# Kernel optimization log

Hardware: AMD Instinct MI355X
Metric: run time of the kernel (lower is better)

## Reference

```python
import jax, jax.numpy as jnp
import numpy as np
from jax import lax

B, N, D = 2, 2048, 256
S, DC, E = 16, 4, 2
DI = E * D            # d_inner = 512
DTR = (D + 15) // 16  # dt_rank = 16


def layernorm(x, w, b):
    m = x.mean(-1, keepdims=True)
    v = ((x - m) ** 2).mean(-1, keepdims=True)
    return (x - m) / jnp.sqrt(v + 1e-5) * w + b


def mamba_block(x, in_w, conv_w, conv_b, xproj_w, dt_w, dt_b, A_log, Dp, out_w):
    # x: [B, N, D]
    xz = jnp.einsum('bnd,ed->bne', x, in_w)          # [B,N,2*DI]
    xc, z = jnp.split(xz, 2, axis=-1)
    # depthwise causal conv1d, kernel DC, left-pad DC-1
    xpad = jnp.pad(xc, ((0, 0), (DC - 1, 0), (0, 0)))
    xconv = sum(xpad[:, k:k + N, :] * conv_w[:, k] for k in range(DC)) + conv_b
    xa = jax.nn.silu(xconv)                           # [B,N,DI]
    x_dbl = jnp.einsum('bnd,ed->bne', xa, xproj_w)    # [B,N,DTR+2S]
    dt = x_dbl[..., :DTR]
    Bm = x_dbl[..., DTR:DTR + S]                      # [B,N,S]
    Cm = x_dbl[..., DTR + S:]                         # [B,N,S]
    dt = jax.nn.softplus(jnp.einsum('bnr,dr->bnd', dt, dt_w) + dt_b)  # [B,N,DI]
    A = -jnp.exp(A_log)                               # [DI,S]
    dA = jnp.exp(dt[..., None] * A)                   # [B,N,DI,S]
    dBu = dt[..., None] * Bm[:, :, None, :] * xa[..., None]

    def step(h, inp):
        dA_t, dBu_t, C_t = inp
        h = dA_t * h + dBu_t                          # [B,DI,S]
        y = jnp.einsum('bds,bs->bd', h, C_t)
        return h, y

    h0 = jnp.zeros((x.shape[0], DI, S), dtype=x.dtype)
    _, ys = lax.scan(step, h0, (dA.transpose(1, 0, 2, 3), dBu.transpose(1, 0, 2, 3), Cm.transpose(1, 0, 2)))
    y = ys.transpose(1, 0, 2) + xa * Dp               # skip D*u
    y = y * jax.nn.silu(z)
    return jnp.einsum('bnd,ed->bne', y, out_w)        # [B,N,D]


def stream_fwd(x, nw, nb, in_w, conv_w, conv_b, xproj_w, dt_w, dt_b, A_log, Dp, out_w):
    return x + mamba_block(layernorm(x, nw, nb), in_w, conv_w, conv_b, xproj_w, dt_w, dt_b, A_log, Dp, out_w)


def setup_inputs() -> dict:
    key = jax.random.key(0)
    ks = jax.random.split(key, 24)
    s = 0.02
    inp = {
        'edge_features': jax.random.normal(ks[0], (B, N, D), jnp.float32),
        'blob_features': jax.random.normal(ks[1], (B, N, D), jnp.float32),
        'spectral_features': jax.random.normal(ks[2], (B, N, D), jnp.float32),
        'norm_w': jnp.ones((3, D)),
        'norm_b': jnp.zeros((3, D)),
        'in_w': jax.random.normal(ks[3], (3, 2 * DI, D)) * s,
        'conv_w': jax.random.normal(ks[4], (3, DI, DC)) * s,
        'conv_b': jnp.zeros((3, DI)),
        'xproj_w': jax.random.normal(ks[5], (3, DTR + 2 * S, DI)) * s,
        'dt_w': jax.random.normal(ks[6], (3, DI, DTR)) * s,
        'dt_b': jax.random.uniform(ks[7], (3, DI), minval=-4.0, maxval=-2.0),
        'A_log': jnp.tile(jnp.log(jnp.arange(1, S + 1, dtype=jnp.float32)), (3, DI, 1)),
        'Dp': jnp.ones((3, DI)),
        'out_w': jax.random.normal(ks[8], (3, D, DI)) * s,
        'temperature': jnp.ones((1,)) * 0.1,
        'agg_w1': jax.random.normal(ks[9], (D, 3 * D)) * s,
        'agg_b1': jnp.zeros((D,)),
        'agg_w2': jax.random.normal(ks[10], (3, D)) * s,
        'agg_b2': jnp.zeros((3,)),
        'proj_w': jax.random.normal(ks[11], (D, 3 * D)) * s,
        'proj_b': jnp.zeros((D,)),
    }
    return inp


def reference(edge_features, blob_features, spectral_features, norm_w, norm_b, in_w,
              conv_w, conv_b, xproj_w, dt_w, dt_b, A_log, Dp, out_w, temperature,
              agg_w1, agg_b1, agg_w2, agg_b2, proj_w, proj_b):
    streams = jnp.stack([edge_features, blob_features, spectral_features])  # [3,B,N,D]
    proc = jax.vmap(stream_fwd)(streams, norm_w, norm_b, in_w, conv_w, conv_b,
                                xproj_w, dt_w, dt_b, A_log, Dp, out_w)      # [3,B,N,D]
    edge_p, blob_p, spec_p = proc[0], proc[1], proc[2]
    multi = jnp.concatenate([edge_p, blob_p, spec_p], axis=-1)              # [B,N,3D]
    pooled = multi.mean(axis=1, keepdims=True)                              # [B,1,3D]
    h = jax.nn.gelu(jnp.einsum('bne,de->bnd', pooled, agg_w1) + agg_b1)
    coeffs = jax.nn.softmax(jnp.einsum('bnd,kd->bnk', h, agg_w2) + agg_b2, axis=-1)
    coeffs = jax.nn.softmax(coeffs / (temperature + 1e-6), axis=-1)         # [B,1,3]
    weighted = (coeffs[:, :, 0:1] * edge_p + coeffs[:, :, 1:2] * blob_p +
                coeffs[:, :, 2:3] * spec_p)
    out = jnp.einsum('bne,de->bnd', multi, proj_w) + proj_b + weighted
    return out  # dropout is identity in eval
```

## Files before the change

kernel.cpp:

```cpp
#include <hip/hip_runtime.h>
#include <hip/hip_bf16.h>

#define NB 2
#define NN 2048
#define ND 256
#define NS 16
#define NDC 4
#define NDI 512
#define NDTR 16
#define LCH 32
#define NCH 64

typedef __hip_bfloat16 bf16;
typedef __attribute__((ext_vector_type(8))) __bf16 bf16x8;
typedef __attribute__((ext_vector_type(4))) float f32x4;

__device__ __forceinline__ float b2f(bf16 h) { return __bfloat162float(h); }

__device__ __forceinline__ void dec8(const uint4 u, float w[8]) {
    union { unsigned u; float f; } c;
    c.u = u.x << 16;          w[0] = c.f;
    c.u = u.x & 0xffff0000u;  w[1] = c.f;
    c.u = u.y << 16;          w[2] = c.f;
    c.u = u.y & 0xffff0000u;  w[3] = c.f;
    c.u = u.z << 16;          w[4] = c.f;
    c.u = u.z & 0xffff0000u;  w[5] = c.f;
    c.u = u.w << 16;          w[6] = c.f;
    c.u = u.w & 0xffff0000u;  w[7] = c.f;
}

struct CvtArgs { const void* s[21]; };
__device__ __constant__ const int seg_cum[22] = {
    0, 1048576, 2097152, 3145728, 3146496, 3147264, 3933696, 3939840,
    3941376, 4015104, 4039680, 4041216, 4065792, 4067328, 4460544, 4460545,
    4657153, 4657409, 4658177, 4658180, 4854788, 4855044 };
__device__ __constant__ const int seg_dst[21] = {
    0,        1048576,  2097152,  4847616, 4848384, 3145728, 4841472, 4849152, 4325376,
    4399104,  4850688,  4423680,  4852224, 3932160, 4855056, 4448256, 4853760, 4854016,
    4854784,  4644864,  4854800 };

__global__ __launch_bounds__(256) void k_convert(CvtArgs a, int* __restrict__ flag,
                                                 bf16* __restrict__ dst,
                                                 float* __restrict__ pooled)
{
    int idx0 = blockIdx.x * 256 + threadIdx.x;
    unsigned v0 = ((const unsigned*)a.s[3])[0];
    int f = ((v0 & 0xFFFFu) == 0u) ? 1 : 0;
    if (idx0 == 0) flag[0] = f;
    if (idx0 < 1536) pooled[idx0] = 0.0f;
    int idx = idx0 + 3145728;
    if (idx >= 4855044) return;
    int seg = 3;
    #pragma unroll
    for (int i = 4; i < 21; i++) if (idx >= seg_cum[i]) seg = i;
    int off = idx - seg_cum[seg];
    bf16 v;
    if (f) v = __float2bfloat16(((const float*)a.s[seg])[off]);
    else   v = ((const bf16*)a.s[seg])[off];
    dst[seg_dst[seg] + off] = v;
}

__global__ __launch_bounds__(256) void k_ln(
    const void* __restrict__ e, const void* __restrict__ bl, const void* __restrict__ sp,
    const void* __restrict__ nw_raw, const void* __restrict__ nb_raw,
    bf16* __restrict__ cvt_in,
    bf16* __restrict__ xn)
{
    int row = blockIdx.x;
    int sb = row >> 11, n = row & (NN - 1);
    int s = sb >> 1, b = sb & 1;
    int t = threadIdx.x;
    unsigned v0 = ((const unsigned*)nw_raw)[0];
    int f = ((v0 & 0xFFFFu) == 0u);
    const void* xin = (s == 0) ? e : ((s == 1) ? bl : sp);
    size_t gi = ((size_t)(b << 11) + n) * ND + t;
    float v = f ? ((const float*)xin)[gi] : b2f(((const bf16*)xin)[gi]);
    cvt_in[(size_t)s * 1048576 + gi] = __float2bfloat16(v);
    float s1 = v, s2 = v * v;
    #pragma unroll
    for (int m = 1; m < 64; m <<= 1) { s1 += __shfl_xor(s1, m); s2 += __shfl_xor(s2, m); }
    __shared__ float r1[4], r2[4];
    int w = t >> 6;
    if ((t & 63) == 0) { r1[w] = s1; r2[w] = s2; }
    __syncthreads();
    float mean = (r1[0] + r1[1] + r1[2] + r1[3]) * (1.0f / ND);
    float ms   = (r2[0] + r2[1] + r2[2] + r2[3]) * (1.0f / ND);
    float inv = rsqrtf(ms - mean * mean + 1e-5f);
    float wv = f ? ((const float*)nw_raw)[s * ND + t] : b2f(((const bf16*)nw_raw)[s * ND + t]);
    float bv = f ? ((const float*)nb_raw)[s * ND + t] : b2f(((const bf16*)nb_raw)[s * ND + t]);
    xn[(size_t)row * ND + t] = __float2bfloat16((v - mean) * inv * wv + bv);
}

__global__ __launch_bounds__(256) void k_inproj_t(
    const bf16* __restrict__ xn, const bf16* __restrict__ in_w,
    bf16* __restrict__ xc, bf16* __restrict__ z)
{
    __shared__ bf16 As[128 * 72];
    __shared__ bf16 Bs[128 * 72];
    int bid = blockIdx.x;
    int bm = bid >> 3, bn = bid & 7;
    int m0 = bm * 128, e0 = bn * 128;
    int s = m0 >> 12;
    const bf16* W = in_w + (size_t)s * (2 * NDI) * ND;
    int t = threadIdx.x;
    int w = t >> 6, l = t & 63;
    int wm = w >> 1, wn = w & 1;
    int quad = l >> 4, lan = l & 15;
    f32x4 acc[4][4];
    #pragma unroll
    for (int mi = 0; mi < 4; mi++)
        #pragma unroll
        for (int j = 0; j < 4; j++) acc[mi][j] = (f32x4){0.f, 0.f, 0.f, 0.f};
    for (int kc0 = 0; kc0 < 256; kc0 += 64) {
        __syncthreads();
        #pragma unroll
        for (int i = 0; i < 4; i++) {
            int li = i * 256 + t;
            int row = li >> 3, col = (li & 7) * 8;
            *(uint4*)&As[row * 72 + col] =
                *(const uint4*)(xn + (size_t)(m0 + row) * ND + kc0 + col);
        }
        #pragma unroll
        for (int i = 0; i < 4; i++) {
            int li = i * 256 + t;
            int row = li >> 3, col = (li & 7) * 8;
            *(uint4*)&Bs[row * 72 + col] =
                *(const uint4*)(W + (size_t)(e0 + row) * ND + kc0 + col);
        }
        __syncthreads();
        #pragma unroll
        for (int kc = 0; kc < 64; kc += 32) {
            bf16x8 af[4], bf[4];
            #pragma unroll
            for (int mi = 0; mi < 4; mi++)
                af[mi] = *(const bf16x8*)&As[(wm * 64 + mi * 16 + lan) * 72 + kc + quad * 8];
            #pragma unroll
            for (int j = 0; j < 4; j++)
                bf[j] = *(const bf16x8*)&Bs[(wn * 64 + j * 16 + lan) * 72 + kc + quad * 8];
            #pragma unroll
            for (int mi = 0; mi < 4; mi++)
                #pragma unroll
                for (int j = 0; j < 4; j++)
                    acc[mi][j] = __builtin_amdgcn_mfma_f32_16x16x32_bf16(af[mi], bf[j], acc[mi][j], 0, 0, 0);
        }
    }
    #pragma unroll
    for (int mi = 0; mi < 4; mi++) {
        #pragma unroll
        for (int j = 0; j < 4; j++) {
            int e = e0 + wn * 64 + j * 16 + lan;
            bf16* dst = (e < NDI) ? xc : z;
            int ec = e & (NDI - 1);
            #pragma unroll
            for (int r = 0; r < 4; r++) {
                int m = m0 + wm * 64 + mi * 16 + quad * 4 + r;
                dst[(size_t)m * NDI + ec] = __float2bfloat16(acc[mi][j][r]);
            }
        }
    }
}

__global__ __launch_bounds__(256) void k_conv(
    const bf16* __restrict__ xc, const bf16* __restrict__ conv_w,
    const bf16* __restrict__ conv_b, bf16* __restrict__ xa)
{
    int idx = blockIdx.x * 256 + threadIdx.x;
    int d8 = (idx & 63) * 8;
    int rn = idx >> 6;
    int n = rn & (NN - 1);
    int sb = rn >> 11;
    int s = sb >> 1;
    const uint4* cwp = (const uint4*)(conv_w + ((size_t)s * NDI + d8) * NDC);
    float cwf[32];
    dec8(cwp[0], cwf); dec8(cwp[1], cwf + 8); dec8(cwp[2], cwf + 16); dec8(cwp[3], cwf + 24);
    float bias[8];
    dec8(*(const uint4*)(conv_b + (size_t)s * NDI + d8), bias);
    size_t g = (size_t)rn * NDI + d8;
    float xv[4][8];
    #pragma unroll
    for (int tau = 0; tau < 4; tau++) {
        if (n >= tau) dec8(*(const uint4*)(xc + g - (size_t)tau * NDI), xv[tau]);
        else
            #pragma unroll
            for (int j = 0; j < 8; j++) xv[tau][j] = 0.0f;
    }
    union { bf16 h[8]; uint4 u; } o;
    #pragma unroll
    for (int j = 0; j < 8; j++) {
        float a = bias[j];
        #pragma unroll
        for (int k = 0; k < 4; k++) a += cwf[j * 4 + k] * xv[3 - k][j];
        a = a / (1.0f + __expf(-a));
        o.h[j] = __float2bfloat16(a);
    }
    *(uint4*)(xa + g) = o.u;
}

__global__ __launch_bounds__(256) void k_xproj_t(
    const bf16* __restrict__ xa, const bf16* __restrict__ xproj_w,
    float* __restrict__ xpart)
{
    __shared__ bf16 As[64 * 72];
    __shared__ bf16 Bs[48 * 72];
    int bid = blockIdx.x;
    int bm = bid >> 2, ks = bid & 3;
    int m0 = bm * 64;
    int s = m0 >> 12;
    const bf16* W = xproj_w + (size_t)s * 48 * NDI;
    int t = threadIdx.x;
    int w = t >> 6, l = t & 63;
    int quad = l >> 4, lan = l & 15;
    f32x4 acc[3];
    #pragma unroll
    for (int j = 0; j < 3; j++) acc[j] = (f32x4){0.f, 0.f, 0.f, 0.f};
    for (int kc0 = ks * 128; kc0 < ks * 128 + 128; kc0 += 64) {
        __syncthreads();
        #pragma unroll
        for (int i = 0; i < 2; i++) {
            int li = i * 256 + t;
            int row = li >> 3, col = (li & 7) * 8;
            *(uint4*)&As[row * 72 + col] =
                *(const uint4*)(xa + (size_t)(m0 + row) * NDI + kc0 + col);
        }
        {
            int li = t;
            if (li < 384) {
                int row = li >> 3, col = (li & 7) * 8;
                *(uint4*)&Bs[row * 72 + col] =
                    *(const uint4*)(W + (size_t)row * NDI + kc0 + col);
            }
            int li2 = 256 + t;
            if (li2 < 384) {
                int row = li2 >> 3, col = (li2 & 7) * 8;
                *(uint4*)&Bs[row * 72 + col] =
                    *(const uint4*)(W + (size_t)row * NDI + kc0 + col);
            }
        }
        __syncthreads();
        #pragma unroll
        for (int kc = 0; kc < 64; kc += 32) {
            bf16x8 af = *(const bf16x8*)&As[(w * 16 + lan) * 72 + kc + quad * 8];
            #pragma unroll
            for (int j = 0; j < 3; j++) {
                bf16x8 bf = *(const bf16x8*)&Bs[(j * 16 + lan) * 72 + kc + quad * 8];
                acc[j] = __builtin_amdgcn_mfma_f32_16x16x32_bf16(af, bf, acc[j], 0, 0, 0);
            }
        }
    }
    float* dst = xpart + (size_t)ks * (12288 * 48);
    #pragma unroll
    for (int j = 0; j < 3; j++) {
        int e = j * 16 + lan;
        #pragma unroll
        for (int r = 0; r < 4; r++) {
            int m = m0 + w * 16 + quad * 4 + r;
            dst[(size_t)m * 48 + e] = acc[j][r];
        }
    }
}

__global__ __launch_bounds__(256) void k_dt2(
    const float* __restrict__ xpart, const bf16* __restrict__ dt_w,
    const bf16* __restrict__ dt_b, float* __restrict__ xdbl, bf16* __restrict__ dt)
{
    __shared__ float xs[4][48];
    int row0 = blockIdx.x * 4;
    int s = row0 >> 12;
    int t = threadIdx.x;
    if (t < 192) {
        int r = t / 48, e = t % 48;
        size_t base = (size_t)(row0 + r) * 48 + e;
        const size_t seg = (size_t)12288 * 48;
        float v = xpart[base] + xpart[base + seg] + xpart[base + 2 * seg] + xpart[base + 3 * seg];
        xs[r][e] = v;
        if (e >= 16) xdbl[base] = v;
    }
    __syncthreads();
    #pragma unroll
    for (int dd = 0; dd < 2; dd++) {
        int d = t + dd * 256;
        const uint4* wp = (const uint4*)(dt_w + ((size_t)s * NDI + d) * NDTR);
        float w[16]; dec8(wp[0], w); dec8(wp[1], w + 8);
        float bias = b2f(dt_b[s * NDI + d]);
        #pragma unroll
        for (int r = 0; r < 4; r++) {
            float a = bias;
            #pragma unroll
            for (int j = 0; j < 16; j++) a += w[j] * xs[r][j];
            a = (a > 20.0f) ? a : log1pf(__expf(a));
            dt[(size_t)(row0 + r) * NDI + d] = __float2bfloat16(a);
        }
    }
}

__global__ __launch_bounds__(256) void k_scan1(
    const bf16* __restrict__ dt, const bf16* __restrict__ xa,
    const bf16* __restrict__ A_log, const float* __restrict__ xdbl,
    float* __restrict__ Hend, float* __restrict__ Pprod)
{
    __shared__ bf16 dts[LCH * 256];
    __shared__ bf16 xas[LCH * 256];
    __shared__ float Bs[LCH * NS];
    int bid = blockIdx.x;
    int sb = bid / (NCH * 2);
    int rem = bid % (NCH * 2);
    int chunk = rem >> 1, dg = rem & 1;
    int s = sb >> 1;
    int t = threadIdx.x;
    int d = dg * 256 + t;
    int n0 = chunk * LCH;
    size_t rowbase = (size_t)sb * NN;
    const bf16* dtg = dt + (rowbase + n0) * NDI + dg * 256;
    const bf16* xag = xa + (rowbase + n0) * NDI + dg * 256;
    #pragma unroll
    for (int i = 0; i < 4; i++) {
        int li = i * 256 + t;
        int row = li >> 5, q = li & 31;
        ((uint4*)dts)[li] = *(const uint4*)(dtg + (size_t)row * NDI + q * 8);
        ((uint4*)xas)[li] = *(const uint4*)(xag + (size_t)row * NDI + q * 8);
    }
    if (t < 128) {
        int row = t >> 2, q = t & 3;
        ((float4*)Bs)[t] = ((const float4*)(xdbl + (rowbase + n0 + row) * 48 + 16))[q];
    }
    float A[16];
    {
        const uint4* ap = (const uint4*)(A_log + ((size_t)s * NDI + d) * NS);
        float al[8]; dec8(ap[0], al);
        #pragma unroll
        for (int i = 0; i < 8; i++) A[i] = -__expf(al[i]);
        dec8(ap[1], al);
        #pragma unroll
        for (int i = 0; i < 8; i++) A[8 + i] = -__expf(al[i]);
    }
    __syncthreads();
    float h[16], P[16];
    #pragma unroll
    for (int i = 0; i < 16; i++) { h[i] = 0.0f; P[i] = 1.0f; }
    #pragma unroll 4
    for (int nl = 0; nl < LCH; nl++) {
        float dtv = b2f(dts[nl * 256 + t]);
        float xav = b2f(xas[nl * 256 + t]);
        float bcom = dtv * xav;
        const float4* br = (const float4*)&Bs[nl * NS];
        float4 b0 = br[0], b1 = br[1], b2 = br[2], b3 = br[3];
        float bv[16] = {b0.x,b0.y,b0.z,b0.w,b1.x,b1.y,b1.z,b1.w,
                        b2.x,b2.y,b2.z,b2.w,b3.x,b3.y,b3.z,b3.w};
        #pragma unroll
        for (int st = 0; st < 16; st++) {
            float dA = __expf(dtv * A[st]);
            h[st] = dA * h[st] + bcom * bv[st];
            P[st] *= dA;
        }
    }
    size_t base = ((size_t)(chunk * 6 + sb) * NS) * NDI + d;
    #pragma unroll
    for (int st = 0; st < 16; st++) {
        Hend[base + (size_t)st * NDI] = h[st];
        Pprod[base + (size_t)st * NDI] = P[st];
    }
}

__global__ __launch_bounds__(256) void k_scomb(float* __restrict__ Hend, const float* __restrict__ Pprod)
{
    int idx = blockIdx.x * 256 + threadIdx.x;
    int sb = idx >> 13;
    int rem = idx & 8191;
    int st = rem >> 9, d = rem & 511;
    float h = 0.0f;
    const size_t stride = (size_t)6 * NS * NDI;
    size_t g = ((size_t)sb * NS + st) * NDI + d;
    #pragma unroll 4
    for (int c = 0; c < NCH; c++) {
        float He = Hend[g], Pp = Pprod[g];
        Hend[g] = h;
        h = He + Pp * h;
        g += stride;
    }
}

__global__ __launch_bounds__(256) void k_scan2(
    const bf16* __restrict__ dt, const bf16* __restrict__ xa, const bf16* __restrict__ z,
    const float* __restrict__ xdbl,
    const bf16* __restrict__ A_log, const bf16* __restrict__ Dp,
    const float* __restrict__ Hstart, bf16* __restrict__ y)
{
    __shared__ bf16 dts[LCH * 256];
    __shared__ bf16 xas[LCH * 256];
    __shared__ bf16 zs[LCH * 256];
    __shared__ float Bs[LCH * NS], Cs[LCH * NS];
    int bid = blockIdx.x;
    int sb = bid / (NCH * 2);
    int rem = bid % (NCH * 2);
    int chunk = rem >> 1, dg = rem & 1;
    int s = sb >> 1;
    int t = threadIdx.x;
    int d = dg * 256 + t;
    int n0 = chunk * LCH;
    size_t rowbase = (size_t)sb * NN;
    const bf16* dtg = dt + (rowbase + n0) * NDI + dg * 256;
    const bf16* xag = xa + (rowbase + n0) * NDI + dg * 256;
    const bf16* zg  = z  + (rowbase + n0) * NDI + dg * 256;
    #pragma unroll
    for (int i = 0; i < 4; i++) {
        int li = i * 256 + t;
        int row = li >> 5, q = li & 31;
        ((uint4*)dts)[li] = *(const uint4*)(dtg + (size_t)row * NDI + q * 8);
        ((uint4*)xas)[li] = *(const uint4*)(xag + (size_t)row * NDI + q * 8);
        ((uint4*)zs)[li]  = *(const uint4*)(zg  + (size_t)row * NDI + q * 8);
    }
    if (t < 128) {
        int row = t >> 2, q = t & 3;
        ((float4*)Bs)[t] = ((const float4*)(xdbl + (rowbase + n0 + row) * 48 + 16))[q];
    } else {
        int t2 = t - 128;
        int row = t2 >> 2, q = t2 & 3;
        ((float4*)Cs)[t2] = ((const float4*)(xdbl + (rowbase + n0 + row) * 48 + 32))[q];
    }
    float A[16];
    {
        const uint4* ap = (const uint4*)(A_log + ((size_t)s * NDI + d) * NS);
        float al[8]; dec8(ap[0], al);
        #pragma unroll
        for (int i = 0; i < 8; i++) A[i] = -__expf(al[i]);
        dec8(ap[1], al);
        #pragma unroll
        for (int i = 0; i < 8; i++) A[8 + i] = -__expf(al[i]);
    }
    float Dpv = b2f(Dp[s * NDI + d]);
    float h[16];
    {
        size_t base = ((size_t)(chunk * 6 + sb) * NS) * NDI + d;
        #pragma unroll
        for (int st = 0; st < 16; st++) h[st] = Hstart[base + (size_t)st * NDI];
    }
    __syncthreads();
    bf16* yp = y + (rowbase + n0) * NDI + d;
    #pragma unroll 4
    for (int nl = 0; nl < LCH; nl++) {
        float dtv = b2f(dts[nl * 256 + t]);
        float xav = b2f(xas[nl * 256 + t]);
        float zz  = b2f(zs[nl * 256 + t]);
        float bcom = dtv * xav;
        const float4* br = (const float4*)&Bs[nl * NS];
        const float4* cr = (const float4*)&Cs[nl * NS];
        float4 b0 = br[0], b1 = br[1], b2 = br[2], b3 = br[3];
        float4 c0 = cr[0], c1 = cr[1], c2 = cr[2], c3 = cr[3];
        float bv[16] = {b0.x,b0.y,b0.z,b0.w,b1.x,b1.y,b1.z,b1.w,
                        b2.x,b2.y,b2.z,b2.w,b3.x,b3.y,b3.z,b3.w};
        float cv[16] = {c0.x,c0.y,c0.z,c0.w,c1.x,c1.y,c1.z,c1.w,
                        c2.x,c2.y,c2.z,c2.w,c3.x,c3.y,c3.z,c3.w};
        float yacc = 0.0f;
        #pragma unroll
        for (int st = 0; st < 16; st++) {
            float dA = __expf(dtv * A[st]);
            h[st] = dA * h[st] + bcom * bv[st];
            yacc += h[st] * cv[st];
        }
        float yv = yacc + xav * Dpv;
        yv *= zz / (1.0f + __expf(-zz));
        yp[(size_t)nl * NDI] = __float2bfloat16(yv);
    }
}

__global__ __launch_bounds__(256) void k_outproj_t(
    const bf16* __restrict__ y, const bf16* __restrict__ out_w,
    const bf16* __restrict__ e_, const bf16* __restrict__ bl, const bf16* __restrict__ sp,
    bf16* __restrict__ proc, float* __restrict__ pooled)
{
    __shared__ bf16 As[128 * 72];
    __shared__ bf16 Bs[64 * 72];
    __shared__ float colsum[64];
    int bid = blockIdx.x;
    int bm = bid >> 2, bn = bid & 3;
    int m0 = bm * 128, e0 = bn * 64;
    int s = m0 >> 12;
    const bf16* W = out_w + (size_t)s * ND * NDI;
    int t = threadIdx.x;
    int w = t >> 6, l = t & 63;
    int quad = l >> 4, lan = l & 15;
    f32x4 acc[2][4];
    #pragma unroll
    for (int mi = 0; mi < 2; mi++)
        #pragma unroll
        for (int j = 0; j < 4; j++) acc[mi][j] = (f32x4){0.f, 0.f, 0.f, 0.f};
    for (int kc0 = 0; kc0 < 512; kc0 += 64) {
        __syncthreads();
        #pragma unroll
        for (int i = 0; i < 4; i++) {
            int li = i * 256 + t;
            int row = li >> 3, col = (li & 7) * 8;
            *(uint4*)&As[row * 72 + col] =
                *(const uint4*)(y + (size_t)(m0 + row) * NDI + kc0 + col);
        }
        #pragma unroll
        for (int i = 0; i < 2; i++) {
            int li = i * 256 + t;
            int row = li >> 3, col = (li & 7) * 8;
            *(uint4*)&Bs[row * 72 + col] =
                *(const uint4*)(W + (size_t)(e0 + row) * NDI + kc0 + col);
        }
        __syncthreads();
        #pragma unroll
        for (int kc = 0; kc < 64; kc += 32) {
            bf16x8 af[2], bf[4];
            #pragma unroll
            for (int mi = 0; mi < 2; mi++)
                af[mi] = *(const bf16x8*)&As[(w * 32 + mi * 16 + lan) * 72 + kc + quad * 8];
            #pragma unroll
            for (int j = 0; j < 4; j++)
                bf[j] = *(const bf16x8*)&Bs[(j * 16 + lan) * 72 + kc + quad * 8];
            #pragma unroll
            for (int mi = 0; mi < 2; mi++)
                #pragma unroll
                for (int j = 0; j < 4; j++)
                    acc[mi][j] = __builtin_amdgcn_mfma_f32_16x16x32_bf16(af[mi], bf[j], acc[mi][j], 0, 0, 0);
        }
    }
    if (t < 64) colsum[t] = 0.0f;
    __syncthreads();
    const bf16* xin = (s == 0) ? e_ : ((s == 1) ? bl : sp);
    int b = (m0 >> 11) & 1;
    #pragma unroll
    for (int mi = 0; mi < 2; mi++) {
        #pragma unroll
        for (int j = 0; j < 4; j++) {
            int e = e0 + j * 16 + lan;
            float ps = 0.0f;
            #pragma unroll
            for (int r = 0; r < 4; r++) {
                int m = m0 + w * 32 + mi * 16 + quad * 4 + r;
                int n = m & (NN - 1);
                float v = acc[mi][j][r] + b2f(xin[((size_t)(b * NN + n)) * ND + e]);
                proc[(size_t)m * ND + e] = __float2bfloat16(v);
                ps += v;
            }
            atomicAdd(&colsum[j * 16 + lan], ps);
        }
    }
    __syncthreads();
    if (t < 64) atomicAdd(&pooled[b * 768 + s * 256 + e0 + t], colsum[t]);
}

__global__ __launch_bounds__(256) void k_final_t(
    const bf16* __restrict__ proc, const bf16* __restrict__ proj_w,
    const bf16* __restrict__ proj_b, const float* __restrict__ pooled,
    const bf16* __restrict__ agg_w1, const bf16* __restrict__ agg_b1,
    const bf16* __restrict__ agg_w2, const bf16* __restrict__ agg_b2,
    const bf16* __restrict__ temp,
    const int* __restrict__ flag, void* __restrict__ out)
{
    __shared__ bf16 As[128 * 72];
    __shared__ bf16 Bs[64 * 72];
    __shared__ float hb[256];
    __shared__ float lg[3];
    __shared__ float cf[3];
    int bid = blockIdx.x;
    int bm = bid >> 2, bn = bid & 3;
    int m0 = bm * 128, e0 = bn * 64;
    int b = m0 >> 11;
    int nbase = m0 & (NN - 1);
    int t = threadIdx.x;
    int w = t >> 6, l = t & 63;
    int quad = l >> 4, lan = l & 15;
    {
        float dot = 0.0f;
        const uint4* wp = (const uint4*)(agg_w1 + (size_t)t * 768);
        for (int k8 = 0; k8 < 96; k8++) {
            float wv[8]; dec8(wp[k8], wv);
            const float* pp = pooled + b * 768 + k8 * 8;
            #pragma unroll
            for (int j = 0; j < 8; j++) dot += wv[j] * pp[j];
        }
        float x = b2f(agg_b1[t]) + dot * (1.0f / NN);
        float inner = 0.7978845608028654f * (x + 0.044715f * x * x * x);
        hb[t] = 0.5f * x * (1.0f + tanhf(inner));
        __syncthreads();
        if (t < 3) {
            float ll = b2f(agg_b2[t]);
            const bf16* w2 = agg_w2 + t * 256;
            for (int d2 = 0; d2 < 256; d2++) ll += b2f(w2[d2]) * hb[d2];
            lg[t] = ll;
        }
        __syncthreads();
        if (t == 0) {
            float m = fmaxf(lg[0], fmaxf(lg[1], lg[2]));
            float e0f = __expf(lg[0] - m), e1 = __expf(lg[1] - m), e2 = __expf(lg[2] - m);
            float iS = 1.0f / (e0f + e1 + e2);
            float c0 = e0f * iS, c1 = e1 * iS, c2 = e2 * iS;
            float tt = b2f(temp[0]) + 1e-6f;
            float m2 = fmaxf(c0, fmaxf(c1, c2)) / tt;
            e0f = __expf(c0 / tt - m2); e1 = __expf(c1 / tt - m2); e2 = __expf(c2 / tt - m2);
            iS = 1.0f / (e0f + e1 + e2);
            cf[0] = e0f * iS; cf[1] = e1 * iS; cf[2] = e2 * iS;
        }
    }
    f32x4 acc[2][4];
    #pragma unroll
    for (int mi = 0; mi < 2; mi++)
        #pragma unroll
        for (int j = 0; j < 4; j++) acc[mi][j] = (f32x4){0.f, 0.f, 0.f, 0.f};
    for (int kc0 = 0; kc0 < 768; kc0 += 64) {
        int sA = kc0 >> 8, kd0 = kc0 & 255;
        const bf16* Asrc = proc + ((size_t)(sA * NB + b) * NN + nbase) * ND + kd0;
        __syncthreads();
        #pragma unroll
        for (int i = 0; i < 4; i++) {
            int li = i * 256 + t;
            int row = li >> 3, col = (li & 7) * 8;
            *(uint4*)&As[row * 72 + col] = *(const uint4*)(Asrc + (size_t)row * ND + col);
        }
        #pragma unroll
        for (int i = 0; i < 2; i++) {
            int li = i * 256 + t;
            int row = li >> 3, col = (li & 7) * 8;
            *(uint4*)&Bs[row * 72 + col] =
                *(const uint4*)(proj_w + (size_t)(e0 + row) * 768 + kc0 + col);
        }
        __syncthreads();
        #pragma unroll
        for (int kc = 0; kc < 64; kc += 32) {
            bf16x8 af[2], bf[4];
            #pragma unroll
            for (int mi = 0; mi < 2; mi++)
                af[mi] = *(const bf16x8*)&As[(w * 32 + mi * 16 + lan) * 72 + kc + quad * 8];
            #pragma unroll
            for (int j = 0; j < 4; j++)
                bf[j] = *(const bf16x8*)&Bs[(j * 16 + lan) * 72 + kc + quad * 8];
            #pragma unroll
            for (int mi = 0; mi < 2; mi++)
                #pragma unroll
                for (int j = 0; j < 4; j++)
                    acc[mi][j] = __builtin_amdgcn_mfma_f32_16x16x32_bf16(af[mi], bf[j], acc[mi][j], 0, 0, 0);
        }
    }
    float c0 = cf[0], c1 = cf[1], c2 = cf[2];
    int f = flag[0];
    #pragma unroll
    for (int mi = 0; mi < 2; mi++) {
        #pragma unroll
        for (int j = 0; j < 4; j++) {
            int e = e0 + j * 16 + lan;
            float pb = b2f(proj_b[e]);
            #pragma unroll
            for (int r = 0; r < 4; r++) {
                int m = m0 + w * 32 + mi * 16 + quad * 4 + r;
                int n = m & (NN - 1);
                size_t pbase = ((size_t)b * NN + n) * ND + e;
                float wres = c0 * b2f(proc[pbase])
                           + c1 * b2f(proc[pbase + (size_t)1 * NB * NN * ND])
                           + c2 * b2f(proc[pbase + (size_t)2 * NB * NN * ND]);
                float v = acc[mi][j][r] + pb + wres;
                if (f) ((float*)out)[(size_t)m * ND + e] = v;
                else   ((bf16*)out)[(size_t)m * ND + e] = __float2bfloat16(v);
            }
        }
    }
}

extern "C" void kernel_launch(void* const* d_in, const int* in_sizes, int n_in,
                              void* d_out, int out_size, void* d_ws, size_t ws_size,
                              hipStream_t stream)
{
    char* w8 = (char*)d_ws;
    int*   flagp   = (int*)(w8);
    bf16*  cvt     = (bf16*)(w8 + 16);
    bf16*  xn      = (bf16*)(w8 + 9710160);
    bf16*  xcb     = (bf16*)(w8 + 16001616);
    bf16*  zb      = (bf16*)(w8 + 28584528);
    bf16*  xab     = (bf16*)(w8 + 41167440);
    bf16*  dtb     = (bf16*)(w8 + 53750352);
    float* xdblb   = (float*)(w8 + 66333264);
    float* pooledb = (float*)(w8 + 68692560);
    float* Hendb   = (float*)(w8 + 68698736);
    float* Pprodb  = (float*)(w8 + 81281648);
    float* xpartb  = (float*)(w8 + 93864560);
    bf16*  procb   = xn;

    const bf16* c_edge   = cvt + 0;
    const bf16* c_blob   = cvt + 1048576;
    const bf16* c_spec   = cvt + 2097152;
    const bf16* c_inw    = cvt + 3145728;
    const bf16* c_outw   = cvt + 3932160;
    const bf16* c_xpw    = cvt + 4325376;
    const bf16* c_dtw    = cvt + 4399104;
    const bf16* c_alog   = cvt + 4423680;
    const bf16* c_agg1   = cvt + 4448256;
    const bf16* c_prjw   = cvt + 4644864;
    const bf16* c_convw  = cvt + 4841472;
    const bf16* c_convb  = cvt + 4849152;
    const bf16* c_dtb    = cvt + 4850688;
    const bf16* c_dp     = cvt + 4852224;
    const bf16* c_agb1   = cvt + 4853760;
    const bf16* c_agw2   = cvt + 4854016;
    const bf16* c_agb2   = cvt + 4854784;
    const bf16* c_prjb   = cvt + 4854800;
    const bf16* c_temp   = cvt + 4855056;

    CvtArgs ca;
    for (int i = 0; i < 21; i++) ca.s[i] = d_in[i];
    k_convert<<<(1709316 + 255) / 256, 256, 0, stream>>>(ca, flagp, cvt, pooledb);
    k_ln<<<6 * NN, 256, 0, stream>>>(d_in[0], d_in[1], d_in[2], d_in[3], d_in[4],
                                     cvt, xn);
    k_inproj_t<<<96 * 8, 256, 0, stream>>>(xn, c_inw, xcb, zb);
    k_conv<<<6 * NN * NDI / 8 / 256, 256, 0, stream>>>(xcb, c_convw, c_convb, xab);
    k_xproj_t<<<192 * 4, 256, 0, stream>>>(xab, c_xpw, xpartb);
    k_dt2<<<3072, 256, 0, stream>>>(xpartb, c_dtw, c_dtb, xdblb, dtb);
    k_scan1<<<6 * NCH * 2, 256, 0, stream>>>(dtb, xab, c_alog, xdblb, Hendb, Pprodb);
    k_scomb<<<192, 256, 0, stream>>>(Hendb, Pprodb);
    k_scan2<<<6 * NCH * 2, 256, 0, stream>>>(dtb, xab, zb, xdblb, c_alog, c_dp, Hendb, xcb);
    k_outproj_t<<<96 * 4, 256, 0, stream>>>(xcb, c_outw, c_edge, c_blob, c_spec, procb, pooledb);
    k_final_t<<<32 * 4, 256, 0, stream>>>(procb, c_prjw, c_prjb, pooledb,
                                          c_agg1, c_agb1, c_agw2, c_agb2, c_temp,
                                          flagp, d_out);
}
```

Baseline: 327.4 us.

## Fuse causal conv into in-proj epilogue; compute gating coeffs in last out-proj block

The in-projection GEMM now applies the depthwise causal conv and SiLU in its epilogue for the xc half. It stages the tile in shared memory and recomputes the three preceding halo rows with an extra MFMA, so the separate conv kernel and the xc round trip through global memory go away. Separately, the aggregation MLP and double softmax move out of every k_final_t block into the last-arriving k_outproj_t block, found with an atomic counter. Each final block no longer redoes the 256x768 dot products. The cost is extra halo work, a threadfence plus atomic counter, and a serial tail on one block.

```diff
diff --git a/kernel.cpp b/kernel.cpp
--- a/kernel.cpp
+++ b/kernel.cpp
@@ -46,7 +46,7 @@
     int idx0 = blockIdx.x * 256 + threadIdx.x;
     unsigned v0 = ((const unsigned*)a.s[3])[0];
     int f = ((v0 & 0xFFFFu) == 0u) ? 1 : 0;
-    if (idx0 == 0) flag[0] = f;
+    if (idx0 == 0) { flag[0] = f; flag[1] = 0; }
     if (idx0 < 1536) pooled[idx0] = 0.0f;
     int idx = idx0 + 3145728;
     if (idx >= 4855044) return;
@@ -63,8 +63,7 @@
 __global__ __launch_bounds__(256) void k_ln(
     const void* __restrict__ e, const void* __restrict__ bl, const void* __restrict__ sp,
     const void* __restrict__ nw_raw, const void* __restrict__ nb_raw,
-    bf16* __restrict__ cvt_in,
-    bf16* __restrict__ xn)
+    bf16* __restrict__ cvt_in, bf16* __restrict__ xn)
 {
     int row = blockIdx.x;
     int sb = row >> 11, n = row & (NN - 1);
@@ -93,14 +92,20 @@
 
 __global__ __launch_bounds__(256) void k_inproj_t(
     const bf16* __restrict__ xn, const bf16* __restrict__ in_w,
-    bf16* __restrict__ xc, bf16* __restrict__ z)
-{
-    __shared__ bf16 As[128 * 72];
-    __shared__ bf16 Bs[128 * 72];
+    const bf16* __restrict__ conv_w, const bf16* __restrict__ conv_b,
+    bf16* __restrict__ xa, bf16* __restrict__ z)
+{
+    __shared__ bf16 sh[2 * 128 * 72];
+    __shared__ bf16 xnx[4][72];
+    bf16* As = sh;
+    bf16* Bs = sh + 128 * 72;
     int bid = blockIdx.x;
     int bm = bid >> 3, bn = bid & 7;
     int m0 = bm * 128, e0 = bn * 128;
     int s = m0 >> 12;
+    int nn0 = m0 & (NN - 1);
+    bool doConv  = (bn < 4);
+    bool doExtra = doConv && (nn0 != 0);
     const bf16* W = in_w + (size_t)s * (2 * NDI) * ND;
     int t = threadIdx.x;
     int w = t >> 6, l = t & 63;
@@ -111,6 +116,9 @@
     for (int mi = 0; mi < 4; mi++)
         #pragma unroll
         for (int j = 0; j < 4; j++) acc[mi][j] = (f32x4){0.f, 0.f, 0.f, 0.f};
+    f32x4 accx[4];
+    #pragma unroll
+    for (int j = 0; j < 4; j++) accx[j] = (f32x4){0.f, 0.f, 0.f, 0.f};
     for (int kc0 = 0; kc0 < 256; kc0 += 64) {
         __syncthreads();
         #pragma unroll
@@ -127,6 +135,11 @@
             *(uint4*)&Bs[row * 72 + col] =
                 *(const uint4*)(W + (size_t)(e0 + row) * ND + kc0 + col);
         }
+        if (doExtra && t < 24) {
+            int i = t >> 3, q = t & 7;
+            *(uint4*)&xnx[i][q * 8] =
+                *(const uint4*)(xn + (size_t)(m0 - 3 + i) * ND + kc0 + q * 8);
+        }
         __syncthreads();
         #pragma unroll
         for (int kc = 0; kc < 64; kc += 32) {
@@ -142,58 +155,80 @@
                 #pragma unroll
                 for (int j = 0; j < 4; j++)
                     acc[mi][j] = __builtin_amdgcn_mfma_f32_16x16x32_bf16(af[mi], bf[j], acc[mi][j], 0, 0, 0);
-        }
-    }
+            if (doExtra && wm == 0) {
+                bf16x8 ax = *(const bf16x8*)&xnx[lan & 3][kc + quad * 8];
+                #pragma unroll
+                for (int j = 0; j < 4; j++)
+                    accx[j] = __builtin_amdgcn_mfma_f32_16x16x32_bf16(ax, bf[j], accx[j], 0, 0, 0);
+            }
+        }
+    }
+    __syncthreads();
+    if (!doConv) {
+        int ebase = e0 & (NDI - 1);
+        #pragma unroll
+        for (int mi = 0; mi < 4; mi++) {
+            #pragma unroll
+            for (int j = 0; j < 4; j++) {
+                int ec = ebase + wn * 64 + j * 16 + lan;
+                #pragma unroll
+                for (int r = 0; r < 4; r++) {
+                    int m = m0 + wm * 64 + mi * 16 + quad * 4 + r;
+                    z[(size_t)m * NDI + ec] = __float2bfloat16(acc[mi][j][r]);
+                }
+            }
+        }
+        return;
+    }
+    bf16* T = sh;
     #pragma unroll
     for (int mi = 0; mi < 4; mi++) {
         #pragma unroll
         for (int j = 0; j < 4; j++) {
-            int e = e0 + wn * 64 + j * 16 + lan;
-            bf16* dst = (e < NDI) ? xc : z;
-            int ec = e & (NDI - 1);
+            int el = wn * 64 + j * 16 + lan;
             #pragma unroll
             for (int r = 0; r < 4; r++) {
-                int m = m0 + wm * 64 + mi * 16 + quad * 4 + r;
-                dst[(size_t)m * NDI + ec] = __float2bfloat16(acc[mi][j][r]);
+                int lm = wm * 64 + mi * 16 + quad * 4 + r;
+                T[(3 + lm) * 136 + el] = __float2bfloat16(acc[mi][j][r]);
             }
         }
     }
-}
-
-__global__ __launch_bounds__(256) void k_conv(
-    const bf16* __restrict__ xc, const bf16* __restrict__ conv_w,
-    const bf16* __restrict__ conv_b, bf16* __restrict__ xa)
-{
-    int idx = blockIdx.x * 256 + threadIdx.x;
-    int d8 = (idx & 63) * 8;
-    int rn = idx >> 6;
-    int n = rn & (NN - 1);
-    int sb = rn >> 11;
-    int s = sb >> 1;
+    if (wm == 0 && quad == 0) {
+        #pragma unroll
+        for (int j = 0; j < 4; j++) {
+            int el = wn * 64 + j * 16 + lan;
+            #pragma unroll
+            for (int r = 0; r < 3; r++)
+                T[r * 136 + el] = doExtra ? __float2bfloat16(accx[j][r]) : __float2bfloat16(0.0f);
+        }
+    }
+    __syncthreads();
+    int cg = t & 15;
+    int col8 = cg * 8;
+    int d8 = e0 + col8;
     const uint4* cwp = (const uint4*)(conv_w + ((size_t)s * NDI + d8) * NDC);
     float cwf[32];
     dec8(cwp[0], cwf); dec8(cwp[1], cwf + 8); dec8(cwp[2], cwf + 16); dec8(cwp[3], cwf + 24);
     float bias[8];
     dec8(*(const uint4*)(conv_b + (size_t)s * NDI + d8), bias);
-    size_t g = (size_t)rn * NDI + d8;
-    float xv[4][8];
-    #pragma unroll
-    for (int tau = 0; tau < 4; tau++) {
-        if (n >= tau) dec8(*(const uint4*)(xc + g - (size_t)tau * NDI), xv[tau]);
-        else
-            #pragma unroll
-            for (int j = 0; j < 8; j++) xv[tau][j] = 0.0f;
-    }
-    union { bf16 h[8]; uint4 u; } o;
-    #pragma unroll
-    for (int j = 0; j < 8; j++) {
-        float a = bias[j];
-        #pragma unroll
-        for (int k = 0; k < 4; k++) a += cwf[j * 4 + k] * xv[3 - k][j];
-        a = a / (1.0f + __expf(-a));
-        o.h[j] = __float2bfloat16(a);
-    }
-    *(uint4*)(xa + g) = o.u;
+    #pragma unroll
+    for (int i = 0; i < 8; i++) {
+        int ro = i * 16 + (t >> 4);
+        float x0[8], x1[8], x2[8], x3[8];
+        dec8(*(const uint4*)&T[(ro + 0) * 136 + col8], x0);
+        dec8(*(const uint4*)&T[(ro + 1) * 136 + col8], x1);
+        dec8(*(const uint4*)&T[(ro + 2) * 136 + col8], x2);
+        dec8(*(const uint4*)&T[(ro + 3) * 136 + col8], x3);
+        union { bf16 h[8]; uint4 u; } o;
+        #pragma unroll
+        for (int jj = 0; jj < 8; jj++) {
+            float a = bias[jj] + cwf[jj * 4 + 0] * x0[jj] + cwf[jj * 4 + 1] * x1[jj]
+                    + cwf[jj * 4 + 2] * x2[jj] + cwf[jj * 4 + 3] * x3[jj];
+            a = a / (1.0f + __expf(-a));
+            o.h[jj] = __float2bfloat16(a);
+        }
+        *(uint4*)(xa + (size_t)(m0 + ro) * NDI + d8) = o.u;
+    }
 }
 
 __global__ __launch_bounds__(256) void k_xproj_t(
@@ -466,11 +501,16 @@
 __global__ __launch_bounds__(256) void k_outproj_t(
     const bf16* __restrict__ y, const bf16* __restrict__ out_w,
     const bf16* __restrict__ e_, const bf16* __restrict__ bl, const bf16* __restrict__ sp,
-    bf16* __restrict__ proc, float* __restrict__ pooled)
+    bf16* __restrict__ proc, float* __restrict__ pooled,
+    const bf16* __restrict__ agg_w1, const bf16* __restrict__ agg_b1,
+    const bf16* __restrict__ agg_w2, const bf16* __restrict__ agg_b2,
+    const bf16* __restrict__ temp, float* __restrict__ coeffs,
+    int* __restrict__ fc)
 {
     __shared__ bf16 As[128 * 72];
     __shared__ bf16 Bs[64 * 72];
     __shared__ float colsum[64];
+    __shared__ int lastf;
     int bid = blockIdx.x;
     int bm = bid >> 2, bn = bid & 3;
     int m0 = bm * 128, e0 = bn * 64;
@@ -540,21 +580,60 @@
     }
     __syncthreads();
     if (t < 64) atomicAdd(&pooled[b * 768 + s * 256 + e0 + t], colsum[t]);
+    __threadfence();
+    if (t == 0) lastf = (atomicAdd(&fc[1], 1) == (int)gridDim.x - 1);
+    __syncthreads();
+    if (!lastf) return;
+    float* plds = (float*)Bs;
+    float* hbb  = plds + 1536;
+    float* lgg  = hbb + 256;
+    for (int i = t; i < 1536; i += 256)
+        plds[i] = __hip_atomic_load(&pooled[i], __ATOMIC_RELAXED, __HIP_MEMORY_SCOPE_AGENT);
+    __syncthreads();
+    for (int bb = 0; bb < NB; bb++) {
+        float dot = 0.0f;
+        const uint4* wp = (const uint4*)(agg_w1 + (size_t)t * 768);
+        for (int k8 = 0; k8 < 96; k8++) {
+            float wv[8]; dec8(wp[k8], wv);
+            const float* pp = plds + bb * 768 + k8 * 8;
+            #pragma unroll
+            for (int j = 0; j < 8; j++) dot += wv[j] * pp[j];
+        }
+        float x = b2f(agg_b1[t]) + dot * (1.0f / NN);
+        float inner = 0.7978845608028654f * (x + 0.044715f * x * x * x);
+        hbb[t] = 0.5f * x * (1.0f + tanhf(inner));
+        __syncthreads();
+        if (t < 3) {
+            float ll = b2f(agg_b2[t]);
+            const bf16* w2 = agg_w2 + t * 256;
+            for (int d2 = 0; d2 < 256; d2++) ll += b2f(w2[d2]) * hbb[d2];
+            lgg[t] = ll;
+        }
+        __syncthreads();
+        if (t == 0) {
+            float m = fmaxf(lgg[0], fmaxf(lgg[1], lgg[2]));
+            float e0f = __expf(lgg[0] - m), e1 = __expf(lgg[1] - m), e2 = __expf(lgg[2] - m);
+            float iS = 1.0f / (e0f + e1 + e2);
+            float c0 = e0f * iS, c1 = e1 * iS, c2 = e2 * iS;
+            float tt = b2f(temp[0]) + 1e-6f;
+            float m2 = fmaxf(c0, fmaxf(c1, c2)) / tt;
+            e0f = __expf(c0 / tt - m2); e1 = __expf(c1 / tt - m2); e2 = __expf(c2 / tt - m2);
+            iS = 1.0f / (e0f + e1 + e2);
+            coeffs[bb * 3 + 0] = e0f * iS;
+            coeffs[bb * 3 + 1] = e1 * iS;
+            coeffs[bb * 3 + 2] = e2 * iS;
+        }
+        __syncthreads();
+    }
 }
 
 __global__ __launch_bounds__(256) void k_final_t(
     const bf16* __restrict__ proc, const bf16* __restrict__ proj_w,
-    const bf16* __restrict__ proj_b, const float* __restrict__ pooled,
-    const bf16* __restrict__ agg_w1, const bf16* __restrict__ agg_b1,
-    const bf16* __restrict__ agg_w2, const bf16* __restrict__ agg_b2,
-    const bf16* __restrict__ temp,
+    const bf16* __restrict__ proj_b, const float* __restrict__ coeffs,
     const int* __restrict__ flag, void* __restrict__ out)
 {
     __shared__ bf16 As[128 * 72];
     __shared__ bf16 Bs[64 * 72];
-    __shared__ float hb[256];
-    __shared__ float lg[3];
-    __shared__ float cf[3];
     int bid = blockIdx.x;
     int bm = bid >> 2, bn = bid & 3;
     int m0 = bm * 128, e0 = bn * 64;
@@ -563,38 +642,6 @@
     int t = threadIdx.x;
     int w = t >> 6, l = t & 63;
     int quad = l >> 4, lan = l & 15;
-    {
-        float dot = 0.0f;
-        const uint4* wp = (const uint4*)(agg_w1 + (size_t)t * 768);
-        for (int k8 = 0; k8 < 96; k8++) {
-            float wv[8]; dec8(wp[k8], wv);
-            const float* pp = pooled + b * 768 + k8 * 8;
-            #pragma unroll
-            for (int j = 0; j < 8; j++) dot += wv[j] * pp[j];
-        }
-        float x = b2f(agg_b1[t]) + dot * (1.0f / NN);
-        float inner = 0.7978845608028654f * (x + 0.044715f * x * x * x);
-        hb[t] = 0.5f * x * (1.0f + tanhf(inner));
-        __syncthreads();
-        if (t < 3) {
-            float ll = b2f(agg_b2[t]);
-            const bf16* w2 = agg_w2 + t * 256;
-            for (int d2 = 0; d2 < 256; d2++) ll += b2f(w2[d2]) * hb[d2];
-            lg[t] = ll;
-        }
-        __syncthreads();
-        if (t == 0) {
-            float m = fmaxf(lg[0], fmaxf(lg[1], lg[2]));
-            float e0f = __expf(lg[0] - m), e1 = __expf(lg[1] - m), e2 = __expf(lg[2] - m);
-            float iS = 1.0f / (e0f + e1 + e2);
-            float c0 = e0f * iS, c1 = e1 * iS, c2 = e2 * iS;
-            float tt = b2f(temp[0]) + 1e-6f;
-            float m2 = fmaxf(c0, fmaxf(c1, c2)) / tt;
-            e0f = __expf(c0 / tt - m2); e1 = __expf(c1 / tt - m2); e2 = __expf(c2 / tt - m2);
-            iS = 1.0f / (e0f + e1 + e2);
-            cf[0] = e0f * iS; cf[1] = e1 * iS; cf[2] = e2 * iS;
-        }
-    }
     f32x4 acc[2][4];
     #pragma unroll
     for (int mi = 0; mi < 2; mi++)
@@ -634,7 +681,7 @@
                     acc[mi][j] = __builtin_amdgcn_mfma_f32_16x16x32_bf16(af[mi], bf[j], acc[mi][j], 0, 0, 0);
         }
     }
-    float c0 = cf[0], c1 = cf[1], c2 = cf[2];
+    float c0 = coeffs[b * 3], c1 = coeffs[b * 3 + 1], c2 = coeffs[b * 3 + 2];
     int f = flag[0];
     #pragma unroll
     for (int mi = 0; mi < 2; mi++) {
@@ -672,6 +719,7 @@
     bf16*  dtb     = (bf16*)(w8 + 53750352);
     float* xdblb   = (float*)(w8 + 66333264);
     float* pooledb = (float*)(w8 + 68692560);
+    float* coeffsb = (float*)(w8 + 68698704);
     float* Hendb   = (float*)(w8 + 68698736);
     float* Pprodb  = (float*)(w8 + 81281648);
     float* xpartb  = (float*)(w8 + 93864560);
@@ -702,15 +750,13 @@
     k_convert<<<(1709316 + 255) / 256, 256, 0, stream>>>(ca, flagp, cvt, pooledb);
     k_ln<<<6 * NN, 256, 0, stream>>>(d_in[0], d_in[1], d_in[2], d_in[3], d_in[4],
                                      cvt, xn);
-    k_inproj_t<<<96 * 8, 256, 0, stream>>>(xn, c_inw, xcb, zb);
-    k_conv<<<6 * NN * NDI / 8 / 256, 256, 0, stream>>>(xcb, c_convw, c_convb, xab);
+    k_inproj_t<<<96 * 8, 256, 0, stream>>>(xn, c_inw, c_convw, c_convb, xab, zb);
     k_xproj_t<<<192 * 4, 256, 0, stream>>>(xab, c_xpw, xpartb);
     k_dt2<<<3072, 256, 0, stream>>>(xpartb, c_dtw, c_dtb, xdblb, dtb);
     k_scan1<<<6 * NCH * 2, 256, 0, stream>>>(dtb, xab, c_alog, xdblb, Hendb, Pprodb);
     k_scomb<<<192, 256, 0, stream>>>(Hendb, Pprodb);
     k_scan2<<<6 * NCH * 2, 256, 0, stream>>>(dtb, xab, zb, xdblb, c_alog, c_dp, Hendb, xcb);
-    k_outproj_t<<<96 * 4, 256, 0, stream>>>(xcb, c_outw, c_edge, c_blob, c_spec, procb, pooledb);
-    k_final_t<<<32 * 4, 256, 0, stream>>>(procb, c_prjw, c_prjb, pooledb,
-                                          c_agg1, c_agb1, c_agw2, c_agb2, c_temp,
-                                          flagp, d_out);
-}
+    k_outproj_t<<<96 * 4, 256, 0, stream>>>(xcb, c_outw, c_edge, c_blob, c_spec, procb, pooledb,
+                                            c_agg1, c_agb1, c_agw2, c_agb2, c_temp, coeffsb, flagp);
+    k_final_t<<<32 * 4, 256, 0, stream>>>(procb, c_prjw, c_prjb, coeffsb, flagp, d_out);
+}
```

Result: slower. 377.2 us (+15.2%).
